# Kernel optimization log

Measured on AMD Instinct MI355X. Metric: run time of the kernel, lower is better.

Reference implementation:

```python
import jax, jax.numpy as jnp
import numpy as np

MAX_LEN = 4
NUM_HEADS = 8
FEAT_DIM = 64
B, N, E = 16, 128, 4096


def setup_inputs() -> dict:
    key = jax.random.key(0)
    k1, k2, k3, k4 = jax.random.split(key, 4)
    edge_feat = jax.random.normal(k1, (B, E, FEAT_DIM), dtype=jnp.float32)
    # path indices in [0, E]; index E selects the appended zero pad row
    path = jax.random.randint(k2, (B, N, N, MAX_LEN), 0, E + 1, dtype=jnp.int32)
    dist = jax.random.randint(k3, (B, N, N), 0, 8, dtype=jnp.int32)
    emb_weight = jax.random.normal(k4, (MAX_LEN * NUM_HEADS, FEAT_DIM), dtype=jnp.float32)
    return {"edge_feat": edge_feat, "path": path, "dist": dist, "emb_weight": emb_weight}


def reference(edge_feat, path, dist, emb_weight):
    b, e, d = edge_feat.shape
    L = path.shape[-1]
    H = NUM_HEADS
    # append zero pad row per graph (index e), as in the torch code
    edata = jnp.concatenate([edge_feat, jnp.zeros((b, 1, d), edge_feat.dtype)], axis=1)  # [B,E+1,d]
    # per-graph gather of edge features along paths: [B,N,N,L,d]
    path_data = jax.vmap(lambda ed, p: ed[p])(edata, path)
    # embedding table restricted to first L*H rows, reshaped [L,H,d]
    emb = emb_weight[: L * H].reshape(L, H, d)
    out = jnp.einsum("bxyld,lhd->bxyh", path_data, emb)  # [B,N,N,H]
    denom = jnp.clip(dist, 1, L).astype(out.dtype)
    return out / denom[..., None]
```

## Files before the change

kernel.cpp:

```cpp
#include <hip/hip_runtime.h>


#define E_DIM 4096
#define D_DIM 64
#define L_DIM 4
#define H_DIM 8
#define LH 32
#define B_DIM 16
#define NN 16384
#define ROWS_PER_B (E_DIM + 1)

typedef float f32x4 __attribute__((ext_vector_type(4)));
typedef int   i32x4 __attribute__((ext_vector_type(4)));
typedef unsigned int u32;

__device__ __forceinline__ u32 f32_bits(float f) { return __builtin_bit_cast(u32, f); }
__device__ __forceinline__ float bits_f32(u32 u) { return __builtin_bit_cast(float, u); }

__device__ __forceinline__ u32 f2bf(float f) {
    u32 x = f32_bits(f);
    return (x + 0x7fffu + ((x >> 16) & 1u)) >> 16;
}

__global__ __launch_bounds__(256) void proj_kernel(
    const float* __restrict__ edge_feat,
    const float* __restrict__ W,
    unsigned short* __restrict__ proj)
{
    const int b     = blockIdx.x & 15;
    const int chunk = blockIdx.x >> 4;
    const int e     = chunk * 256 + threadIdx.x;
    if (e > E_DIM) return;
    const int r = b * ROWS_PER_B + e;

    i32x4* outp = (i32x4*)(proj + (size_t)r * LH);

    if (e == E_DIM) {
        i32x4 z = (i32x4)0;
        #pragma unroll
        for (int q = 0; q < 4; ++q) outp[q] = z;
        return;
    }

    const f32x4* row4 = (const f32x4*)(edge_feat + ((size_t)b * E_DIM + e) * D_DIM);
    f32x4 row[16];
    #pragma unroll
    for (int i = 0; i < 16; ++i) row[i] = row4[i];

    const f32x4* W4 = (const f32x4*)W;

    u32 packed[16];
    for (int jq = 0; jq < 8; ++jq) {
        float tmp[4];
        #pragma unroll
        for (int jj = 0; jj < 4; ++jj) {
            const int j = jq * 4 + jj;
            f32x4 acc = (f32x4)0.f;
            #pragma unroll
            for (int d4 = 0; d4 < 16; ++d4) {
                acc += row[d4] * W4[j * 16 + d4];
            }
            tmp[jj] = (acc.x + acc.y) + (acc.z + acc.w);
        }
        packed[jq * 2]     = f2bf(tmp[0]) | (f2bf(tmp[1]) << 16);
        packed[jq * 2 + 1] = f2bf(tmp[2]) | (f2bf(tmp[3]) << 16);
    }
    #pragma unroll
    for (int q = 0; q < 4; ++q) {
        i32x4 v = { (int)packed[q*4], (int)packed[q*4+1], (int)packed[q*4+2], (int)packed[q*4+3] };
        outp[q] = v;
    }
}

__global__ __launch_bounds__(256) void gather_kernel(
    const i32x4* __restrict__ path4,
    const int*  __restrict__ dist,
    const unsigned short* __restrict__ proj,
    float* __restrict__ out)
{
    const int tid   = threadIdx.x;
    const int blk   = blockIdx.x;
    const int b     = blk & 15;
    const int chunk = blk >> 4;
    const int gid   = (b << 14) | (chunk << 8) | tid;

    i32x4 p = __builtin_nontemporal_load(path4 + gid);
    int  dv = __builtin_nontemporal_load(dist + gid);

    const unsigned short* pb = proj + (size_t)b * ROWS_PER_B * LH;

    i32x4 A = *(const i32x4*)(pb + (u32)p.x * LH + 0);
    i32x4 Bv= *(const i32x4*)(pb + (u32)p.y * LH + 8);
    i32x4 C = *(const i32x4*)(pb + (u32)p.z * LH + 16);
    i32x4 D = *(const i32x4*)(pb + (u32)p.w * LH + 24);

    dv = dv < 1 ? 1 : (dv > L_DIM ? L_DIM : dv);
    float s = 1.0f / (float)dv;

    float oo[8];
    #pragma unroll
    for (int k = 0; k < 4; ++k) {
        u32 a = (u32)A[k], bb = (u32)Bv[k], c = (u32)C[k], d = (u32)D[k];
        float fe = (bits_f32(a << 16) + bits_f32(bb << 16))
                 + (bits_f32(c << 16) + bits_f32(d << 16));
        float fo = (bits_f32(a & 0xffff0000u) + bits_f32(bb & 0xffff0000u))
                 + (bits_f32(c & 0xffff0000u) + bits_f32(d & 0xffff0000u));
        oo[2*k]   = fe * s;
        oo[2*k+1] = fo * s;
    }
    f32x4 o0 = { oo[0], oo[1], oo[2], oo[3] };
    f32x4 o1 = { oo[4], oo[5], oo[6], oo[7] };

    f32x4* op = (f32x4*)(out + (size_t)gid * 8);
    __builtin_nontemporal_store(o0, op);
    __builtin_nontemporal_store(o1, op + 1);
}

extern "C" void kernel_launch(void* const* d_in, const int* in_sizes, int n_in,
                              void* d_out, int out_size, void* d_ws, size_t ws_size,
                              hipStream_t stream) {
    const float* edge_feat = (const float*)d_in[0];
    const int*   path      = (const int*)  d_in[1];
    const int*   dist      = (const int*)  d_in[2];
    const float* emb_w     = (const float*)d_in[3];

    unsigned short* proj = (unsigned short*)d_ws;

    proj_kernel<<<17 * B_DIM, 256, 0, stream>>>(edge_feat, emb_w, proj);

    gather_kernel<<<(B_DIM * NN) / 256, 256, 0, stream>>>(
        (const i32x4*)path, dist, proj, (float*)d_out);
}
```

Baseline: 90.40 us.

## Restructure projection kernel: stage W in LDS, split output heads across waves

The projection kernel now loads the 32x64 embedding weight into shared memory once per block. Each wave computes 8 of the 32 output channels for 64 rows, with each thread handling 4 rows. Rows are linearized across batches, so the grid is packed tightly instead of launching a partly idle chunk per batch. This aims to cut redundant global weight reads and per-thread register pressure from holding a full 64-float row. In exchange, each edge row is reloaded by all four waves, and index math gains divisions.

```diff
diff --git a/kernel.cpp b/kernel.cpp
--- a/kernel.cpp
+++ b/kernel.cpp
@@ -9,6 +9,7 @@
 #define B_DIM 16
 #define NN 16384
 #define ROWS_PER_B (E_DIM + 1)
+#define TOTAL_ROWS (B_DIM * ROWS_PER_B)
 
 typedef float f32x4 __attribute__((ext_vector_type(4)));
 typedef int   i32x4 __attribute__((ext_vector_type(4)));
@@ -27,48 +28,73 @@
     const float* __restrict__ W,
     unsigned short* __restrict__ proj)
 {
-    const int b     = blockIdx.x & 15;
-    const int chunk = blockIdx.x >> 4;
-    const int e     = chunk * 256 + threadIdx.x;
-    if (e > E_DIM) return;
-    const int r = b * ROWS_PER_B + e;
+    __shared__ f32x4 Wl[LH * 16];
 
-    i32x4* outp = (i32x4*)(proj + (size_t)r * LH);
+    const int tid = threadIdx.x;
+    const f32x4* W4 = (const f32x4*)W;
+    Wl[tid]       = W4[tid];
+    Wl[tid + 256] = W4[tid + 256];
+    __syncthreads();
 
-    if (e == E_DIM) {
-        i32x4 z = (i32x4)0;
-        #pragma unroll
-        for (int q = 0; q < 4; ++q) outp[q] = z;
-        return;
+    const int w    = tid >> 6;
+    const int l    = tid & 63;
+    const int base = blockIdx.x * 256;
+
+    int  r[4];
+    bool valid[4], pad[4];
+    size_t rowbase[4];
+    #pragma unroll
+    for (int i = 0; i < 4; ++i) {
+        r[i]     = base + l + i * 64;
+        valid[i] = r[i] < TOTAL_ROWS;
+        int bi   = valid[i] ? (r[i] / ROWS_PER_B) : 0;
+        int ei   = valid[i] ? (r[i] - bi * ROWS_PER_B) : 0;
+        pad[i]   = (ei == E_DIM);
+        rowbase[i] = valid[i] ? ((size_t)bi * E_DIM + (pad[i] ? 0 : ei)) * D_DIM : 0;
     }
 
-    const f32x4* row4 = (const f32x4*)(edge_feat + ((size_t)b * E_DIM + e) * D_DIM);
-    f32x4 row[16];
+    float acc[4][8];
     #pragma unroll
-    for (int i = 0; i < 16; ++i) row[i] = row4[i];
+    for (int i = 0; i < 4; ++i)
+        #pragma unroll
+        for (int jj = 0; jj < 8; ++jj) acc[i][jj] = 0.f;
 
-    const f32x4* W4 = (const f32x4*)W;
+    for (int c = 0; c < 4; ++c) {
+        f32x4 rowc[4][4];
+        #pragma unroll
+        for (int i = 0; i < 4; ++i) {
+            const f32x4* src = (const f32x4*)(edge_feat + rowbase[i] + c * 16);
+            #pragma unroll
+            for (int q = 0; q < 4; ++q) rowc[i][q] = src[q];
+        }
+        #pragma unroll
+        for (int jj = 0; jj < 8; ++jj) {
+            const int j = w * 8 + jj;
+            f32x4 w0 = Wl[j * 16 + c * 4 + 0];
+            f32x4 w1 = Wl[j * 16 + c * 4 + 1];
+            f32x4 w2 = Wl[j * 16 + c * 4 + 2];
+            f32x4 w3 = Wl[j * 16 + c * 4 + 3];
+            #pragma unroll
+            for (int i = 0; i < 4; ++i) {
+                f32x4 t = rowc[i][0] * w0;
+                t += rowc[i][1] * w1;
+                t += rowc[i][2] * w2;
+                t += rowc[i][3] * w3;
+                acc[i][jj] += (t.x + t.y) + (t.z + t.w);
+            }
+        }
+    }
 
-    u32 packed[16];
-    for (int jq = 0; jq < 8; ++jq) {
-        float tmp[4];
-        #pragma unroll
-        for (int jj = 0; jj < 4; ++jj) {
-            const int j = jq * 4 + jj;
-            f32x4 acc = (f32x4)0.f;
-            #pragma unroll
-            for (int d4 = 0; d4 < 16; ++d4) {
-                acc += row[d4] * W4[j * 16 + d4];
-            }
-            tmp[jj] = (acc.x + acc.y) + (acc.z + acc.w);
-        }
-        packed[jq * 2]     = f2bf(tmp[0]) | (f2bf(tmp[1]) << 16);
-        packed[jq * 2 + 1] = f2bf(tmp[2]) | (f2bf(tmp[3]) << 16);
-    }
     #pragma unroll
-    for (int q = 0; q < 4; ++q) {
-        i32x4 v = { (int)packed[q*4], (int)packed[q*4+1], (int)packed[q*4+2], (int)packed[q*4+3] };
-        outp[q] = v;
+    for (int i = 0; i < 4; ++i) {
+        if (!valid[i]) continue;
+        u32 p0 = f2bf(acc[i][0]) | (f2bf(acc[i][1]) << 16);
+        u32 p1 = f2bf(acc[i][2]) | (f2bf(acc[i][3]) << 16);
+        u32 p2 = f2bf(acc[i][4]) | (f2bf(acc[i][5]) << 16);
+        u32 p3 = f2bf(acc[i][6]) | (f2bf(acc[i][7]) << 16);
+        if (pad[i]) { p0 = p1 = p2 = p3 = 0u; }
+        i32x4 v = { (int)p0, (int)p1, (int)p2, (int)p3 };
+        *(i32x4*)(proj + (size_t)r[i] * LH + w * 8) = v;
     }
 }
 
@@ -126,7 +152,7 @@
 
     unsigned short* proj = (unsigned short*)d_ws;
 
-    proj_kernel<<<17 * B_DIM, 256, 0, stream>>>(edge_feat, emb_w, proj);
+    proj_kernel<<<(TOTAL_ROWS + 255) / 256, 256, 0, stream>>>(edge_feat, emb_w, proj);
 
     gather_kernel<<<(B_DIM * NN) / 256, 256, 0, stream>>>(
         (const i32x4*)path, dist, proj, (float*)d_out);
```

Result: slower. 195.3 us (+116.1%).

## Split projection across four threads per row and stage weights in LDS

Applied to the files above, without the earlier changes.

The projection kernel now assigns four threads per edge row, each computing 8 of the 32 outputs, instead of one thread per row. This gives 4x more blocks (about 1025) for the 256-CU device. The weight matrix is staged into shared memory with padding to avoid bank conflicts, replacing repeated global or scalar loads. The cost is that each row of edge features is loaded by four threads redundantly, which relies on cache hits, and there is extra sync overhead.

```diff
diff --git a/kernel.cpp b/kernel.cpp
--- a/kernel.cpp
+++ b/kernel.cpp
@@ -9,6 +9,7 @@
 #define B_DIM 16
 #define NN 16384
 #define ROWS_PER_B (E_DIM + 1)
+#define TOTAL_ROWS (B_DIM * ROWS_PER_B)
 
 typedef float f32x4 __attribute__((ext_vector_type(4)));
 typedef int   i32x4 __attribute__((ext_vector_type(4)));
@@ -27,18 +28,29 @@
     const float* __restrict__ W,
     unsigned short* __restrict__ proj)
 {
-    const int b     = blockIdx.x & 15;
-    const int chunk = blockIdx.x >> 4;
-    const int e     = chunk * 256 + threadIdx.x;
-    if (e > E_DIM) return;
-    const int r = b * ROWS_PER_B + e;
+    __shared__ f32x4 Wl[LH * 16 + 4];
 
-    i32x4* outp = (i32x4*)(proj + (size_t)r * LH);
+    const int tid = threadIdx.x;
+    const f32x4* W4 = (const f32x4*)W;
+    {
+        int i0 = tid;
+        int i1 = tid + 256;
+        Wl[i0 + (i0 >> 7)] = W4[i0];
+        Wl[i1 + (i1 >> 7)] = W4[i1];
+    }
+    __syncthreads();
+
+    const int js = tid & 3;
+    const int rl = tid >> 2;
+    const int r  = blockIdx.x * 64 + rl;
+    if (r >= TOTAL_ROWS) return;
+    const int b = r / ROWS_PER_B;
+    const int e = r - b * ROWS_PER_B;
+
+    i32x4* outp = (i32x4*)(proj + (size_t)r * LH + js * 8);
 
     if (e == E_DIM) {
-        i32x4 z = (i32x4)0;
-        #pragma unroll
-        for (int q = 0; q < 4; ++q) outp[q] = z;
+        *outp = (i32x4)0;
         return;
     }
 
@@ -47,29 +59,24 @@
     #pragma unroll
     for (int i = 0; i < 16; ++i) row[i] = row4[i];
 
-    const f32x4* W4 = (const f32x4*)W;
-
-    u32 packed[16];
-    for (int jq = 0; jq < 8; ++jq) {
-        float tmp[4];
+    const int jbase = js * 8;
+    u32 pk[4];
+    #pragma unroll
+    for (int jp = 0; jp < 4; ++jp) {
+        const int j0 = jbase + jp * 2;
+        const int j1 = j0 + 1;
+        f32x4 a0 = (f32x4)0.f, a1 = (f32x4)0.f;
         #pragma unroll
-        for (int jj = 0; jj < 4; ++jj) {
-            const int j = jq * 4 + jj;
-            f32x4 acc = (f32x4)0.f;
-            #pragma unroll
-            for (int d4 = 0; d4 < 16; ++d4) {
-                acc += row[d4] * W4[j * 16 + d4];
-            }
-            tmp[jj] = (acc.x + acc.y) + (acc.z + acc.w);
+        for (int d4 = 0; d4 < 16; ++d4) {
+            a0 += row[d4] * Wl[j0 * 16 + d4 + js];
+            a1 += row[d4] * Wl[j1 * 16 + d4 + js];
         }
-        packed[jq * 2]     = f2bf(tmp[0]) | (f2bf(tmp[1]) << 16);
-        packed[jq * 2 + 1] = f2bf(tmp[2]) | (f2bf(tmp[3]) << 16);
+        float s0 = (a0.x + a0.y) + (a0.z + a0.w);
+        float s1 = (a1.x + a1.y) + (a1.z + a1.w);
+        pk[jp] = f2bf(s0) | (f2bf(s1) << 16);
     }
-    #pragma unroll
-    for (int q = 0; q < 4; ++q) {
-        i32x4 v = { (int)packed[q*4], (int)packed[q*4+1], (int)packed[q*4+2], (int)packed[q*4+3] };
-        outp[q] = v;
-    }
+    i32x4 v = { (int)pk[0], (int)pk[1], (int)pk[2], (int)pk[3] };
+    *outp = v;
 }
 
 __global__ __launch_bounds__(256) void gather_kernel(
@@ -126,7 +133,7 @@
 
     unsigned short* proj = (unsigned short*)d_ws;
 
-    proj_kernel<<<17 * B_DIM, 256, 0, stream>>>(edge_feat, emb_w, proj);
+    proj_kernel<<<(TOTAL_ROWS + 63) / 64, 256, 0, stream>>>(edge_feat, emb_w, proj);
 
     gather_kernel<<<(B_DIM * NN) / 256, 256, 0, stream>>>(
         (const i32x4*)path, dist, proj, (float*)d_out);
```

After: 83.34 us. 7.8% less time.

## Compute edge projection with bf16 MFMA tiles instead of scalar FMA loops

Applied to the files above, without the earlier changes.

Rewrites the projection kernel so each wave computes 16-row tiles of edge_feat x W^T using mfma_f32_16x16x32_bf16, with the inputs converted to bf16 in registers. The old version had each thread do 32x64 scalar FMAs per row, making the projection compute-bound and limited to 272 blocks. The new version launches 513 blocks with up to two tiles per wave. In exchange, the inputs are rounded to bf16 before the matmul, which lowers accuracy, and the outputs are written as scattered 2-byte stores.

```diff
diff --git a/kernel.cpp b/kernel.cpp
--- a/kernel.cpp
+++ b/kernel.cpp
@@ -9,9 +9,14 @@
 #define B_DIM 16
 #define NN 16384
 #define ROWS_PER_B (E_DIM + 1)
+#define TOTAL_ROWS (B_DIM * ROWS_PER_B)
+#define N_TILES (TOTAL_ROWS / 16)
+#define P1_BLOCKS 513
+#define P1_WAVES (P1_BLOCKS * 4)
 
 typedef float f32x4 __attribute__((ext_vector_type(4)));
 typedef int   i32x4 __attribute__((ext_vector_type(4)));
+typedef short s16x8 __attribute__((ext_vector_type(8)));
 typedef unsigned int u32;
 
 __device__ __forceinline__ u32 f32_bits(float f) { return __builtin_bit_cast(u32, f); }
@@ -22,53 +27,67 @@
     return (x + 0x7fffu + ((x >> 16) & 1u)) >> 16;
 }
 
+__device__ __forceinline__ s16x8 pack_bf16x8(f32x4 lo, f32x4 hi) {
+    u32 q0 = f2bf(lo.x) | (f2bf(lo.y) << 16);
+    u32 q1 = f2bf(lo.z) | (f2bf(lo.w) << 16);
+    u32 q2 = f2bf(hi.x) | (f2bf(hi.y) << 16);
+    u32 q3 = f2bf(hi.z) | (f2bf(hi.w) << 16);
+    i32x4 q = { (int)q0, (int)q1, (int)q2, (int)q3 };
+    return __builtin_bit_cast(s16x8, q);
+}
+
 __global__ __launch_bounds__(256) void proj_kernel(
     const float* __restrict__ edge_feat,
     const float* __restrict__ W,
     unsigned short* __restrict__ proj)
 {
-    const int b     = blockIdx.x & 15;
-    const int chunk = blockIdx.x >> 4;
-    const int e     = chunk * 256 + threadIdx.x;
-    if (e > E_DIM) return;
-    const int r = b * ROWS_PER_B + e;
+    const int wid  = threadIdx.x >> 6;
+    const int lane = threadIdx.x & 63;
+    const int wgid = blockIdx.x * 4 + wid;
+    const int lr   = lane & 15;
+    const int k0   = (lane >> 4) * 8;
 
-    i32x4* outp = (i32x4*)(proj + (size_t)r * LH);
+    s16x8 bf[2][2];
+    #pragma unroll
+    for (int jt = 0; jt < 2; ++jt)
+        #pragma unroll
+        for (int kt = 0; kt < 2; ++kt) {
+            const float* ws = W + (jt * 16 + lr) * 64 + kt * 32 + k0;
+            bf[jt][kt] = pack_bf16x8(*(const f32x4*)ws, *(const f32x4*)(ws + 4));
+        }
 
-    if (e == E_DIM) {
-        i32x4 z = (i32x4)0;
+    #pragma unroll
+    for (int tt = 0; tt < 2; ++tt) {
+        const int tile = wgid + tt * P1_WAVES;
+        if (tile >= N_TILES) break;
+        const int row0 = tile * 16;
+
+        int ra = row0 + lr;
+        int ba = ra / ROWS_PER_B;
+        int ea = ra - ba * ROWS_PER_B;
+        if (ea == E_DIM) ea = 0;
+        const float* as = edge_feat + ((size_t)ba * E_DIM + ea) * D_DIM + k0;
+        s16x8 af0 = pack_bf16x8(*(const f32x4*)as,        *(const f32x4*)(as + 4));
+        s16x8 af1 = pack_bf16x8(*(const f32x4*)(as + 32), *(const f32x4*)(as + 36));
+
+        f32x4 acc0 = (f32x4)0.f, acc1 = (f32x4)0.f;
+        acc0 = __builtin_amdgcn_mfma_f32_16x16x32_bf16(af0, bf[0][0], acc0, 0, 0, 0);
+        acc0 = __builtin_amdgcn_mfma_f32_16x16x32_bf16(af1, bf[0][1], acc0, 0, 0, 0);
+        acc1 = __builtin_amdgcn_mfma_f32_16x16x32_bf16(af0, bf[1][0], acc1, 0, 0, 0);
+        acc1 = __builtin_amdgcn_mfma_f32_16x16x32_bf16(af1, bf[1][1], acc1, 0, 0, 0);
+
+        const int rbase = row0 + (lane >> 4) * 4;
         #pragma unroll
-        for (int q = 0; q < 4; ++q) outp[q] = z;
-        return;
-    }
-
-    const f32x4* row4 = (const f32x4*)(edge_feat + ((size_t)b * E_DIM + e) * D_DIM);
-    f32x4 row[16];
-    #pragma unroll
-    for (int i = 0; i < 16; ++i) row[i] = row4[i];
-
-    const f32x4* W4 = (const f32x4*)W;
-
-    u32 packed[16];
-    for (int jq = 0; jq < 8; ++jq) {
-        float tmp[4];
-        #pragma unroll
-        for (int jj = 0; jj < 4; ++jj) {
-            const int j = jq * 4 + jj;
-            f32x4 acc = (f32x4)0.f;
-            #pragma unroll
-            for (int d4 = 0; d4 < 16; ++d4) {
-                acc += row[d4] * W4[j * 16 + d4];
-            }
-            tmp[jj] = (acc.x + acc.y) + (acc.z + acc.w);
+        for (int reg = 0; reg < 4; ++reg) {
+            int rg = rbase + reg;
+            int bg = rg / ROWS_PER_B;
+            int eg = rg - bg * ROWS_PER_B;
+            unsigned short v0 = (unsigned short)f2bf(acc0[reg]);
+            unsigned short v1 = (unsigned short)f2bf(acc1[reg]);
+            if (eg == E_DIM) { v0 = 0; v1 = 0; }
+            proj[(size_t)rg * LH + lr]      = v0;
+            proj[(size_t)rg * LH + 16 + lr] = v1;
         }
-        packed[jq * 2]     = f2bf(tmp[0]) | (f2bf(tmp[1]) << 16);
-        packed[jq * 2 + 1] = f2bf(tmp[2]) | (f2bf(tmp[3]) << 16);
-    }
-    #pragma unroll
-    for (int q = 0; q < 4; ++q) {
-        i32x4 v = { (int)packed[q*4], (int)packed[q*4+1], (int)packed[q*4+2], (int)packed[q*4+3] };
-        outp[q] = v;
     }
 }
 
@@ -126,7 +145,7 @@
 
     unsigned short* proj = (unsigned short*)d_ws;
 
-    proj_kernel<<<17 * B_DIM, 256, 0, stream>>>(edge_feat, emb_w, proj);
+    proj_kernel<<<P1_BLOCKS, 256, 0, stream>>>(edge_feat, emb_w, proj);
 
     gather_kernel<<<(B_DIM * NN) / 256, 256, 0, stream>>>(
         (const i32x4*)path, dist, proj, (float*)d_out);
```

After: 80.78 us. 10.6% less time.
